# Optimization experiments

Measured on AMD Instinct MI355X. Metric: run time of the kernel, lower is better.

The kernel has to match this reference:

```python
import jax, jax.numpy as jnp
import numpy as np

FEAT_STRIDE = 16
NEG_THR, POS_THR = 0.3, 0.7        # cfg.TRAIN.RPN_NEGATIVE_OVERLAP / RPN_POSITIVE_OVERLAP
RPN_BATCHSIZE, NUM_FG = 256, 128   # RPN_BATCHSIZE, FG_FRACTION=0.5
A_PER_LOC = 9


def generate_anchors(base_size=16, ratios=(0.5, 1.0, 2.0), scales=(8, 16, 32)):
    w = h = float(base_size)
    xc = yc = 0.5 * (base_size - 1)
    size = w * h
    ws = np.round(np.sqrt(size / np.array(ratios)))
    hs = np.round(ws * np.array(ratios))
    out = []
    for wi, hi in zip(ws, hs):
        for s in scales:
            W, H = wi * s, hi * s
            out.append([xc - 0.5 * (W - 1), yc - 0.5 * (H - 1),
                        xc + 0.5 * (W - 1), yc + 0.5 * (H - 1)])
    return np.array(out, dtype=np.float32)  # [9, 4]


def _forward(rpn_cls_score, gt_boxes, im_info):
    B, _, H, W = rpn_cls_score.shape
    A = A_PER_LOC
    base = jnp.asarray(generate_anchors())
    sx, sy = jnp.meshgrid(jnp.arange(W) * FEAT_STRIDE, jnp.arange(H) * FEAT_STRIDE)  # 'xy', [H,W]
    shifts = jnp.stack([sx.ravel(), sy.ravel(), sx.ravel(), sy.ravel()], 1).astype(jnp.float32)  # [K,4]
    anchors = (base[None, :, :] + shifts[:, None, :]).reshape(-1, 4)  # [N=K*A, 4], (h,w,a)-major
    N = anchors.shape[0]

    img_h, img_w = im_info[0, 0], im_info[0, 1]
    inside = ((anchors[:, 0] >= 0) & (anchors[:, 1] >= 0) &
              (anchors[:, 2] < img_w) & (anchors[:, 3] < img_h))  # [N]

    # ---- IoU overlaps (torch +1 pixel convention) ----
    gt = gt_boxes[..., :4]  # [B,Kg,4]
    aw = anchors[:, 2] - anchors[:, 0] + 1.0
    ah = anchors[:, 3] - anchors[:, 1] + 1.0
    a_area = aw * ah                                   # [N]
    g_area = (gt[..., 2] - gt[..., 0] + 1.0) * (gt[..., 3] - gt[..., 1] + 1.0)  # [B,Kg]
    ix = jnp.maximum(0.0, jnp.minimum(anchors[None, :, None, 2], gt[:, None, :, 2])
                     - jnp.maximum(anchors[None, :, None, 0], gt[:, None, :, 0]) + 1.0)
    iy = jnp.maximum(0.0, jnp.minimum(anchors[None, :, None, 3], gt[:, None, :, 3])
                     - jnp.maximum(anchors[None, :, None, 1], gt[:, None, :, 1]) + 1.0)
    inter = ix * iy
    ovr = inter / (a_area[None, :, None] + g_area[:, None, :] - inter)  # [B,N,Kg]

    max_ovr = ovr.max(2)
    arg = ovr.argmax(2)                                 # [B,N]
    ovr_in = jnp.where(inside[None, :, None], ovr, 0.0)  # only in-image anchors compete for gt-max
    gt_max = ovr_in.max(1)                              # [B,Kg]
    gt_max = jnp.where(gt_max == 0.0, 1e-5, gt_max)
    is_best = (ovr_in == gt_max[:, None, :]).any(2)     # [B,N]

    # ---- label assignment (RPN_CLOBBER_POSITIVES = False) ----
    lbl = jnp.full((B, N), -1.0, jnp.float32)
    lbl = jnp.where(inside[None] & (max_ovr < NEG_THR), 0.0, lbl)
    lbl = jnp.where(inside[None] & is_best, 1.0, lbl)
    lbl = jnp.where(inside[None] & (max_ovr >= POS_THR), 1.0, lbl)

    # ---- random fg/bg subsampling (deterministic jax PRNG replaces np.random.permutation) ----
    def _subsample(lbl_b, key):
        kf, kb = jax.random.split(key)
        def disable(l, mask, limit, k):
            prio = jnp.where(mask, jax.random.uniform(k, l.shape), -1.0)
            order = jnp.argsort(-prio)
            rank = jnp.zeros(l.shape[0], jnp.int32).at[order].set(jnp.arange(l.shape[0], dtype=jnp.int32))
            return jnp.where(mask & (rank >= limit), -1.0, l)
        lbl_b = disable(lbl_b, lbl_b == 1.0, NUM_FG, kf)
        num_bg = RPN_BATCHSIZE - jnp.sum(lbl_b == 1.0)
        return disable(lbl_b, lbl_b == 0.0, num_bg, kb)

    lbl = jax.vmap(_subsample)(lbl, jax.random.split(jax.random.key(42), B))

    assigned = jnp.take_along_axis(gt, arg[..., None], axis=1)  # [B,N,4]
    acx = anchors[:, 0] + 0.5 * (aw - 1.0)
    acy = anchors[:, 1] + 0.5 * (ah - 1.0)
    g_w = assigned[..., 2] - assigned[..., 0] + 1.0
    g_h = assigned[..., 3] - assigned[..., 1] + 1.0
    gcx = assigned[..., 0] + 0.5 * (g_w - 1.0)
    gcy = assigned[..., 1] + 0.5 * (g_h - 1.0)
    targets = jnp.stack([(gcx - acx[None]) / aw[None], (gcy - acy[None]) / ah[None],
                         jnp.log(g_w / aw[None]), jnp.log(g_h / ah[None])], -1)  # [B,N,4]

    in_w = jnp.where(lbl == 1.0, 1.0, 0.0)             # RPN_BBOX_INSIDE_WEIGHTS = 1
    num_examples = jnp.sum(lbl >= 0.0, axis=1).astype(jnp.float32)  # RPN_POSITIVE_WEIGHT = -1
    uw = 1.0 / num_examples                             # uniform pos/neg weight, per batch
    out_w = jnp.where((lbl == 1.0) | (lbl == 0.0), uw[:, None], 0.0)

    # ---- _unmap with fill=0 for out-of-image anchors ----
    lbl = jnp.where(inside[None], lbl, 0.0)
    targets = jnp.where(inside[None, :, None], targets, 0.0)
    in_w = jnp.where(inside[None], in_w, 0.0)
    out_w = jnp.where(inside[None], out_w, 0.0)

    labels_out = lbl.reshape(B, H, W, A).transpose(0, 3, 1, 2).reshape(B, 1, A * H, W)
    targets_out = targets.reshape(B, H, W, 4 * A).transpose(0, 3, 1, 2)
    in_w_out = jnp.broadcast_to(in_w[..., None], (B, N, 4)).reshape(B, H, W, 4 * A).transpose(0, 3, 1, 2)
    out_w_out = jnp.broadcast_to(out_w[..., None], (B, N, 4)).reshape(B, H, W, 4 * A).transpose(0, 3, 1, 2)
    return labels_out, targets_out, in_w_out, out_w_out


def setup_inputs() -> dict:
    key = jax.random.key(0)
    B, A, H, W, Kg = 16, 9, 64, 64, 50
    k1, k2, k3, k4, k5 = jax.random.split(key, 5)
    rpn_cls_score = jax.random.normal(k1, (B, 2 * A, H, W), jnp.float32)
    # valid GT boxes inside a 1024x1024 image, class label in column 4
    x1 = jax.random.uniform(k2, (B, Kg)) * 800.0
    y1 = jax.random.uniform(k3, (B, Kg)) * 800.0
    w = 20.0 + jax.random.uniform(k4, (B, Kg)) * 200.0
    h = 20.0 + jax.random.uniform(k5, (B, Kg)) * 200.0
    cls = jnp.ones((B, Kg), jnp.float32)
    gt_boxes = jnp.stack([x1, y1, x1 + w, y1 + h, cls], -1)
    im_info = jnp.full((B, 2), 1024.0, jnp.float32)
    return {"rpn_cls_score": rpn_cls_score, "gt_boxes": gt_boxes, "im_info": im_info, "num_boxes": Kg}


def reference(rpn_cls_score, gt_boxes, im_info, num_boxes):
    return _forward(rpn_cls_score, gt_boxes, im_info)
```

## Files before the change

kernel.cpp:

```cpp
#include <hip/hip_runtime.h>
#include <stdint.h>


#define B_   16
#define A_   9
#define H_   64
#define W_   64
#define HW_  (H_*W_)
#define N_   (HW_*A_)
#define KG_  50
#define S0_  (B_*A_*HW_)
#define S1_  (B_*4*A_*HW_)
#define NGTB_ (B_*KG_)
#define CAP_  20480
#define NHIST_ (B_*2*256 + B_*2)

typedef unsigned long long ull;

__constant__ float c_base[A_][4] = {
  { -84.f,  -40.f,  99.f,  55.f},
  {-176.f,  -88.f, 191.f, 103.f},
  {-360.f, -184.f, 375.f, 199.f},
  { -56.f,  -56.f,  71.f,  71.f},
  {-120.f, -120.f, 135.f, 135.f},
  {-248.f, -248.f, 263.f, 263.f},
  { -36.f,  -80.f,  51.f,  95.f},
  { -80.f, -168.f,  95.f, 183.f},
  {-168.f, -344.f, 183.f, 359.f},
};

__device__ __forceinline__ void tf2x32(uint32_t k0, uint32_t k1,
                                       uint32_t x0, uint32_t x1,
                                       uint32_t& o0, uint32_t& o1) {
  const uint32_t ks2 = k0 ^ k1 ^ 0x1BD11BDAu;
  uint32_t ks[3] = {k0, k1, ks2};
  x0 += ks[0]; x1 += ks[1];
  const int R[2][4] = {{13,15,26,6},{17,29,16,24}};
  #pragma unroll
  for (int i = 0; i < 5; i++) {
    #pragma unroll
    for (int j = 0; j < 4; j++) {
      x0 += x1;
      int r = R[i & 1][j];
      x1 = (x1 << r) | (x1 >> (32 - r));
      x1 ^= x0;
    }
    x0 += ks[(i + 1) % 3];
    x1 += ks[(i + 2) % 3] + (uint32_t)(i + 1);
  }
  o0 = x0; o1 = x1;
}

__device__ __attribute__((noinline))
float box_area_f(float x1, float y1, float x2, float y2) {
#pragma clang fp contract(off)
  return (x2 - x1 + 1.f) * (y2 - y1 + 1.f);
}

__device__ __attribute__((noinline))
float iou_core(float ax1, float ay1, float ax2, float ay2, float aarea,
               float gx1, float gy1, float gx2, float gy2, float garea) {
#pragma clang fp contract(off)
  float ix = fmaxf(fminf(ax2, gx2) - fmaxf(ax1, gx1) + 1.f, 0.f);
  float iy = fmaxf(fminf(ay2, gy2) - fmaxf(ay1, gy1) + 1.f, 0.f);
  float inter = ix * iy;
  return inter / (aarea + garea - inter);
}

__global__ __launch_bounds__(256) void k_gtmax(const float* __restrict__ gtb,
                                               const float* __restrict__ iminfo,
                                               float* __restrict__ gt_max,
                                               uint32_t* __restrict__ keys,
                                               int* __restrict__ cnt_hist) {
  const int b = blockIdx.x / KG_;
  const int g = blockIdx.x % KG_;
  const int tid = threadIdx.x;
  if (blockIdx.x == 0 && tid < B_) {
    uint32_t k0, k1, kf0, kf1, kb0, kb1;
    tf2x32(0u, 42u, 0u, (uint32_t)tid, k0, k1);
    tf2x32(k0, k1, 0u, 0u, kf0, kf1);
    tf2x32(k0, k1, 0u, 1u, kb0, kb1);
    keys[tid * 4 + 0] = kf0;
    keys[tid * 4 + 1] = kf1;
    keys[tid * 4 + 2] = kb0;
    keys[tid * 4 + 3] = kb1;
  }
  if (blockIdx.x < 32) {
    const int per = (NHIST_ + 31) / 32;
    const int base = blockIdx.x * per;
    const int lim = min(base + per, NHIST_);
    for (int i = base + tid; i < lim; i += 256) cnt_hist[i] = 0;
  }
  const float* gp = gtb + (b * KG_ + g) * 5;
  const float gx1 = gp[0], gy1 = gp[1], gx2 = gp[2], gy2 = gp[3];
  const float garea = box_area_f(gx1, gy1, gx2, gy2);
  const float imh = iminfo[0], imw = iminfo[1];
  float best = 0.f;
  for (int a = 0; a < A_; a++) {
    const float bx1 = c_base[a][0], by1 = c_base[a][1];
    const float bx2 = c_base[a][2], by2 = c_base[a][3];
    const float aarea = box_area_f(bx1, by1, bx2, by2);
    int xlo = max(0, (int)ceilf(-bx1 / 16.f));
    int xhi = min(W_ - 1, (int)ceilf((imw - bx2) / 16.f) - 1);
    int ylo = max(0, (int)ceilf(-by1 / 16.f));
    int yhi = min(H_ - 1, (int)ceilf((imh - by2) / 16.f) - 1);
    xlo = max(xlo, (int)floorf((gx1 - 1.f - bx2) / 16.f));
    xhi = min(xhi, (int)ceilf((gx2 + 1.f - bx1) / 16.f));
    ylo = max(ylo, (int)floorf((gy1 - 1.f - by2) / 16.f));
    yhi = min(yhi, (int)ceilf((gy2 + 1.f - by1) / 16.f));
    const int nx = xhi - xlo + 1, ny = yhi - ylo + 1;
    if (nx <= 0 || ny <= 0) continue;
    const int lw = (nx <= 1) ? 0 : (32 - __clz(nx - 1));
    const int tot = ny << lw;
    const int mask = (1 << lw) - 1;
    for (int t = tid; t < tot; t += 256) {
      const int xi = t & mask;
      if (xi >= nx) continue;
      const int x = xlo + xi;
      const int y = ylo + (t >> lw);
      const float sx = 16.f * (float)x, sy = 16.f * (float)y;
      best = fmaxf(best, iou_core(bx1 + sx, by1 + sy, bx2 + sx, by2 + sy,
                                  aarea, gx1, gy1, gx2, gy2, garea));
    }
  }
  best = fmaxf(best, __shfl_xor(best, 32));
  best = fmaxf(best, __shfl_xor(best, 16));
  best = fmaxf(best, __shfl_xor(best, 8));
  best = fmaxf(best, __shfl_xor(best, 4));
  best = fmaxf(best, __shfl_xor(best, 2));
  best = fmaxf(best, __shfl_xor(best, 1));
  __shared__ float sw[4];
  if ((tid & 63) == 0) sw[tid >> 6] = best;
  __syncthreads();
  if (tid == 0)
    gt_max[b * KG_ + g] = fmaxf(fmaxf(sw[0], sw[1]), fmaxf(sw[2], sw[3]));
}

__global__ __launch_bounds__(256) void k_fuse(const float* __restrict__ gtb,
                                              const float* __restrict__ iminfo,
                                              const float* __restrict__ gt_max,
                                              const uint32_t* __restrict__ keys,
                                              float* __restrict__ lbl,
                                              int* __restrict__ amax,
                                              ull* __restrict__ cand,
                                              int* __restrict__ cnt,
                                              int* __restrict__ hist) {
  __shared__ float sgx1[KG_], sgy1[KG_], sgx2[KG_], sgy2[KG_], sga[KG_], sgm[KG_];
  __shared__ int s_xlo[A_], s_ylo[A_], s_nx[A_], s_pre[A_ + 1];
  __shared__ uint32_t s_k[4];
  __shared__ int s_num[2], s_base[2];
  const int b = blockIdx.y;
  const int tid = threadIdx.x;
  if (tid < KG_) {
    const float* g = gtb + (b * KG_ + tid) * 5;
    float x1 = g[0], y1 = g[1], x2 = g[2], y2 = g[3];
    sgx1[tid] = x1; sgy1[tid] = y1; sgx2[tid] = x2; sgy2[tid] = y2;
    sga[tid] = box_area_f(x1, y1, x2, y2);
    float gm = gt_max[b * KG_ + tid];
    sgm[tid] = (gm == 0.f) ? 1e-5f : gm;
  }
  if (tid < 4) s_k[tid] = keys[b * 4 + tid];
  if (tid < 2) s_num[tid] = 0;
  if (tid < A_) {
    const float imh = iminfo[0], imw = iminfo[1];
    const float bx1 = c_base[tid][0], by1 = c_base[tid][1];
    const float bx2 = c_base[tid][2], by2 = c_base[tid][3];
    int xlo = max(0, (int)ceilf(-bx1 / 16.f));
    int xhi = min(W_ - 1, (int)ceilf((imw - bx2) / 16.f) - 1);
    int ylo = max(0, (int)ceilf(-by1 / 16.f));
    int yhi = min(H_ - 1, (int)ceilf((imh - by2) / 16.f) - 1);
    int nx = max(0, xhi - xlo + 1), ny = max(0, yhi - ylo + 1);
    s_xlo[tid] = xlo; s_ylo[tid] = ylo; s_nx[tid] = nx;
    s_pre[tid + 1] = nx * ny;
  }
  __syncthreads();
  if (tid == 0) {
    s_pre[0] = 0;
    for (int a = 0; a < A_; a++) s_pre[a + 1] += s_pre[a];
  }
  __syncthreads();
  const int C = s_pre[A_];
  const int t = blockIdx.x * 256 + tid;

  bool act = false;
  int p = 0, lpos = 0, n = 0;
  uint32_t m = 0;
  if (t < C) {
    int a = 0;
    while (t >= s_pre[a + 1]) a++;
    const int idx = t - s_pre[a];
    const int nx = s_nx[a];
    const int y = s_ylo[a] + idx / nx;
    const int x = s_xlo[a] + (idx - (idx / nx) * nx);
    n = (y * W_ + x) * A_ + a;
    const float sx = 16.f * (float)x, sy = 16.f * (float)y;
    const float ax1 = c_base[a][0] + sx, ay1 = c_base[a][1] + sy;
    const float ax2 = c_base[a][2] + sx, ay2 = c_base[a][3] + sy;
    const float aarea = box_area_f(c_base[a][0], c_base[a][1],
                                   c_base[a][2], c_base[a][3]);
    float mo = -1.f;
    int bidx = 0;
    bool best = false;
    for (int k = 0; k < KG_; k++) {
      float ovr = iou_core(ax1, ay1, ax2, ay2, aarea,
                           sgx1[k], sgy1[k], sgx2[k], sgy2[k], sga[k]);
      if (ovr > mo) { mo = ovr; bidx = k; }
      best = best || (ovr == sgm[k]);
    }
    float l = -1.f;
    if (mo < 0.3f) l = 0.f;
    if (best || mo >= 0.7f) l = 1.f;
    lbl[(size_t)b * N_ + n] = l;
    amax[(size_t)b * N_ + n] = bidx;
    if (l >= 0.f) {
      act = true;
      p = (l == 1.f) ? 0 : 1;
      uint32_t y0, y1;
      tf2x32(s_k[2 * p], s_k[2 * p + 1], 0u, (uint32_t)n, y0, y1);
      m = (y0 ^ y1) >> 9;
      lpos = atomicAdd(&s_num[p], 1);
    }
  }
  __syncthreads();
  if (tid < 2 && s_num[tid] > 0)
    s_base[tid] = atomicAdd(&cnt[b * 2 + tid], s_num[tid]);
  __syncthreads();
  if (act) {
    cand[(size_t)(b * 2 + p) * CAP_ + s_base[p] + lpos] =
        ((ull)m << 16) | (ull)(65535 - n);
    atomicAdd(&hist[(b * 2 + p) * 256 + (int)(m >> 15)], 1);
  }
}

__global__ __launch_bounds__(256) void k_select(const ull* __restrict__ cand,
                                                const int* __restrict__ cnt,
                                                const int* __restrict__ hist,
                                                ull* __restrict__ Kstar,
                                                float* __restrict__ uw) {
  const int b = blockIdx.x >> 1, p = blockIdx.x & 1;
  const int tid = threadIdx.x;
  __shared__ ull s_keys[2048];
  __shared__ int s_bin, s_r, s_n;
  const int cf = cnt[b * 2 + 0], cb = cnt[b * 2 + 1];
  const int limit = (p == 0) ? 128 : 256 - min(cf, 128);
  const int c = (p == 0) ? cf : cb;
  if (p == 1 && tid == 0) {
    int kf = min(cf, 128);
    int kb = min(cb, 256 - kf);
    uw[b] = 1.f / (float)(kf + kb);
  }
  if (c <= limit) {
    if (tid == 0) Kstar[b * 2 + p] = 0ull;
    return;
  }
  if (tid == 0) {
    const int* Hh = hist + (b * 2 + p) * 256;
    int acc = 0, bin = 255, r = 0;
    for (; bin >= 0; bin--) {
      int hv = Hh[bin];
      if (acc + hv >= limit) { r = limit - acc; break; }
      acc += hv;
    }
    s_bin = bin; s_r = r; s_n = 0;
  }
  __syncthreads();
  const uint32_t bin0 = (uint32_t)s_bin;
  const int r0 = s_r;
  const ull* C = cand + (size_t)(b * 2 + p) * CAP_;
  for (int i = tid; i < c; i += 256) {
    ull k = C[i];
    if ((uint32_t)(k >> 31) == bin0) {
      int pos = atomicAdd(&s_n, 1);
      if (pos < 2048) s_keys[pos] = k;
    }
  }
  __syncthreads();
  const int s = min(s_n, 2048);
  for (int j = tid; j < s; j += 256) {
    ull kj = s_keys[j];
    int rank = 0;
    for (int q = 0; q < s; q++) rank += (s_keys[q] > kj) ? 1 : 0;
    if (rank == r0 - 1) Kstar[b * 2 + p] = kj;
  }
}

__global__ __launch_bounds__(256) void k_out(const float* __restrict__ gtb,
                                             const float* __restrict__ iminfo,
                                             const float* __restrict__ lbl,
                                             const int* __restrict__ amax,
                                             const ull* __restrict__ Kstar,
                                             const float* __restrict__ uw,
                                             const uint32_t* __restrict__ keys,
                                             float* __restrict__ out) {
  const int t = blockIdx.x * 256 + threadIdx.x;
  const int w = t & 63;
  const int h = (t >> 6) & 63;
  const int a = (t >> 12) % A_;
  const int b = t / (A_ * HW_);
  const int n = (h * W_ + w) * A_ + a;

  const float ax1 = c_base[a][0] + 16.f * (float)w;
  const float ay1 = c_base[a][1] + 16.f * (float)h;
  const float ax2 = c_base[a][2] + 16.f * (float)w;
  const float ay2 = c_base[a][3] + 16.f * (float)h;
  const float imh = iminfo[0], imw = iminfo[1];
  const bool ins = (ax1 >= 0.f) && (ay1 >= 0.f) && (ax2 < imw) && (ay2 < imh);

  float l = ins ? lbl[(size_t)b * N_ + n] : -1.f;
  if (ins && l >= 0.f) {
    const int p = (l == 1.f) ? 0 : 1;
    uint32_t y0, y1;
    tf2x32(keys[b * 4 + 2 * p], keys[b * 4 + 2 * p + 1], 0u, (uint32_t)n, y0, y1);
    ull key = ((ull)((y0 ^ y1) >> 9) << 16) | (ull)(65535 - n);
    if (key < Kstar[b * 2 + p]) l = -1.f;
  }

  out[(size_t)b * (A_ * HW_) + a * HW_ + h * W_ + w] = ins ? l : 0.f;

  float tx = 0.f, ty = 0.f, tw = 0.f, th = 0.f;
  if (ins) {
    const int g = amax[(size_t)b * N_ + n];
    const float* gp = gtb + ((size_t)b * KG_ + g) * 5;
    float aw = ax2 - ax1 + 1.f, ah = ay2 - ay1 + 1.f;
    float acx = ax1 + 0.5f * (aw - 1.f), acy = ay1 + 0.5f * (ah - 1.f);
    float gw = gp[2] - gp[0] + 1.f, gh = gp[3] - gp[1] + 1.f;
    float gcx = gp[0] + 0.5f * (gw - 1.f), gcy = gp[1] + 0.5f * (gh - 1.f);
    tx = (gcx - acx) / aw;
    ty = (gcy - acy) / ah;
    tw = logf(gw / aw);
    th = logf(gh / ah);
  }
  float* o1 = out + S0_;
  const size_t toff = (size_t)b * (4 * A_ * HW_) + (4 * a) * HW_ + h * W_ + w;
  o1[toff]           = tx;
  o1[toff + HW_]     = ty;
  o1[toff + 2 * HW_] = tw;
  o1[toff + 3 * HW_] = th;

  const float inw = (ins && l == 1.f) ? 1.f : 0.f;
  const float oww = (ins && l >= 0.f) ? uw[b] : 0.f;
  float* o2 = out + S0_ + S1_;
  o2[toff] = inw; o2[toff + HW_] = inw; o2[toff + 2 * HW_] = inw; o2[toff + 3 * HW_] = inw;
  float* o3 = out + S0_ + 2 * (size_t)S1_;
  o3[toff] = oww; o3[toff + HW_] = oww; o3[toff + 2 * HW_] = oww; o3[toff + 3 * HW_] = oww;
}

extern "C" void kernel_launch(void* const* d_in, const int* in_sizes, int n_in,
                              void* d_out, int out_size, void* d_ws, size_t ws_size,
                              hipStream_t stream) {
  const float* gtb = (const float*)d_in[1];
  const float* iminfo = (const float*)d_in[2];
  float* out = (float*)d_out;

  float* lbl = (float*)d_ws;
  int* amax = (int*)(lbl + (size_t)B_ * N_);
  float* gt_max = (float*)(amax + (size_t)B_ * N_);
  float* uw = gt_max + B_ * KG_;
  uint32_t* keys = (uint32_t*)(uw + B_);
  int* cnt = (int*)(keys + B_ * 4);
  int* hist = cnt + B_ * 2;
  ull* Kstar = (ull*)(hist + B_ * 2 * 256);
  ull* cand = Kstar + B_ * 2;

  k_gtmax<<<NGTB_, 256, 0, stream>>>(gtb, iminfo, gt_max, keys, cnt);
  k_fuse<<<dim3(144, B_), 256, 0, stream>>>(gtb, iminfo, gt_max, keys,
                                            lbl, amax, cand, cnt, hist);
  k_select<<<B_ * 2, 256, 0, stream>>>(cand, cnt, hist, Kstar, uw);
  k_out<<<S0_ / 256, 256, 0, stream>>>(gtb, iminfo, lbl, amax, Kstar, uw,
                                       keys, out);
}
```

Baseline: 137.1 us.

## Pack label and argmax into one int and vectorize output kernel with float4

Label and argmax index are packed into a single int array stored in (a,h,w) order, so the intermediate workspace is half as large and the output kernel reads it contiguously. The output kernel now handles four consecutive w positions per thread, loading an int4 and writing float4 stores to all output planes. The fuse kernel becomes a grid-stride loop with fewer blocks (73 per batch instead of 144), which adds a few extra barriers per iteration. Cost: more registers per thread in the output kernel and fewer threads in flight for the IoU stage.

```diff
diff --git a/kernel.cpp b/kernel.cpp
--- a/kernel.cpp
+++ b/kernel.cpp
@@ -140,8 +140,7 @@
                                               const float* __restrict__ iminfo,
                                               const float* __restrict__ gt_max,
                                               const uint32_t* __restrict__ keys,
-                                              float* __restrict__ lbl,
-                                              int* __restrict__ amax,
+                                              int* __restrict__ packed,
                                               ull* __restrict__ cand,
                                               int* __restrict__ cnt,
                                               int* __restrict__ hist) {
@@ -160,7 +159,6 @@
     sgm[tid] = (gm == 0.f) ? 1e-5f : gm;
   }
   if (tid < 4) s_k[tid] = keys[b * 4 + tid];
-  if (tid < 2) s_num[tid] = 0;
   if (tid < A_) {
     const float imh = iminfo[0], imw = iminfo[1];
     const float bx1 = c_base[tid][0], by1 = c_base[tid][1];
@@ -180,55 +178,61 @@
   }
   __syncthreads();
   const int C = s_pre[A_];
-  const int t = blockIdx.x * 256 + tid;
-
-  bool act = false;
-  int p = 0, lpos = 0, n = 0;
-  uint32_t m = 0;
-  if (t < C) {
-    int a = 0;
-    while (t >= s_pre[a + 1]) a++;
-    const int idx = t - s_pre[a];
-    const int nx = s_nx[a];
-    const int y = s_ylo[a] + idx / nx;
-    const int x = s_xlo[a] + (idx - (idx / nx) * nx);
-    n = (y * W_ + x) * A_ + a;
-    const float sx = 16.f * (float)x, sy = 16.f * (float)y;
-    const float ax1 = c_base[a][0] + sx, ay1 = c_base[a][1] + sy;
-    const float ax2 = c_base[a][2] + sx, ay2 = c_base[a][3] + sy;
-    const float aarea = box_area_f(c_base[a][0], c_base[a][1],
-                                   c_base[a][2], c_base[a][3]);
-    float mo = -1.f;
-    int bidx = 0;
-    bool best = false;
-    for (int k = 0; k < KG_; k++) {
-      float ovr = iou_core(ax1, ay1, ax2, ay2, aarea,
-                           sgx1[k], sgy1[k], sgx2[k], sgy2[k], sga[k]);
-      if (ovr > mo) { mo = ovr; bidx = k; }
-      best = best || (ovr == sgm[k]);
-    }
-    float l = -1.f;
-    if (mo < 0.3f) l = 0.f;
-    if (best || mo >= 0.7f) l = 1.f;
-    lbl[(size_t)b * N_ + n] = l;
-    amax[(size_t)b * N_ + n] = bidx;
-    if (l >= 0.f) {
-      act = true;
-      p = (l == 1.f) ? 0 : 1;
-      uint32_t y0, y1;
-      tf2x32(s_k[2 * p], s_k[2 * p + 1], 0u, (uint32_t)n, y0, y1);
-      m = (y0 ^ y1) >> 9;
-      lpos = atomicAdd(&s_num[p], 1);
-    }
-  }
-  __syncthreads();
-  if (tid < 2 && s_num[tid] > 0)
-    s_base[tid] = atomicAdd(&cnt[b * 2 + tid], s_num[tid]);
-  __syncthreads();
-  if (act) {
-    cand[(size_t)(b * 2 + p) * CAP_ + s_base[p] + lpos] =
-        ((ull)m << 16) | (ull)(65535 - n);
-    atomicAdd(&hist[(b * 2 + p) * 256 + (int)(m >> 15)], 1);
+  const int stride = gridDim.x * 256;
+
+  for (int t0 = blockIdx.x * 256; t0 < C; t0 += stride) {
+    if (tid < 2) s_num[tid] = 0;
+    __syncthreads();
+    const int t = t0 + tid;
+    bool act = false;
+    int p = 0, lpos = 0, n = 0;
+    uint32_t m = 0;
+    if (t < C) {
+      int a = 0;
+      while (t >= s_pre[a + 1]) a++;
+      const int idx = t - s_pre[a];
+      const int nx = s_nx[a];
+      const int y = s_ylo[a] + idx / nx;
+      const int x = s_xlo[a] + (idx - (idx / nx) * nx);
+      n = (y * W_ + x) * A_ + a;
+      const int n2 = a * HW_ + y * W_ + x;
+      const float sx = 16.f * (float)x, sy = 16.f * (float)y;
+      const float ax1 = c_base[a][0] + sx, ay1 = c_base[a][1] + sy;
+      const float ax2 = c_base[a][2] + sx, ay2 = c_base[a][3] + sy;
+      const float aarea = box_area_f(c_base[a][0], c_base[a][1],
+                                     c_base[a][2], c_base[a][3]);
+      float mo = -1.f;
+      int bidx = 0;
+      bool best = false;
+      for (int k = 0; k < KG_; k++) {
+        float ovr = iou_core(ax1, ay1, ax2, ay2, aarea,
+                             sgx1[k], sgy1[k], sgx2[k], sgy2[k], sga[k]);
+        if (ovr > mo) { mo = ovr; bidx = k; }
+        best = best || (ovr == sgm[k]);
+      }
+      int lab = -1;
+      if (mo < 0.3f) lab = 0;
+      if (best || mo >= 0.7f) lab = 1;
+      packed[(size_t)b * N_ + n2] = (bidx << 2) | (lab + 1);
+      if (lab >= 0) {
+        act = true;
+        p = (lab == 1) ? 0 : 1;
+        uint32_t y0, y1;
+        tf2x32(s_k[2 * p], s_k[2 * p + 1], 0u, (uint32_t)n, y0, y1);
+        m = (y0 ^ y1) >> 9;
+        lpos = atomicAdd(&s_num[p], 1);
+      }
+    }
+    __syncthreads();
+    if (tid < 2 && s_num[tid] > 0)
+      s_base[tid] = atomicAdd(&cnt[b * 2 + tid], s_num[tid]);
+    __syncthreads();
+    if (act) {
+      cand[(size_t)(b * 2 + p) * CAP_ + s_base[p] + lpos] =
+          ((ull)m << 16) | (ull)(65535 - n);
+      atomicAdd(&hist[(b * 2 + p) * 256 + (int)(m >> 15)], 1);
+    }
+    __syncthreads();
   }
 }
 
@@ -286,63 +290,88 @@
 
 __global__ __launch_bounds__(256) void k_out(const float* __restrict__ gtb,
                                              const float* __restrict__ iminfo,
-                                             const float* __restrict__ lbl,
-                                             const int* __restrict__ amax,
+                                             const int* __restrict__ packed,
                                              const ull* __restrict__ Kstar,
                                              const float* __restrict__ uw,
                                              const uint32_t* __restrict__ keys,
                                              float* __restrict__ out) {
-  const int t = blockIdx.x * 256 + threadIdx.x;
-  const int w = t & 63;
-  const int h = (t >> 6) & 63;
-  const int a = (t >> 12) % A_;
-  const int b = t / (A_ * HW_);
-  const int n = (h * W_ + w) * A_ + a;
-
-  const float ax1 = c_base[a][0] + 16.f * (float)w;
+  const int gid = blockIdx.x * 256 + threadIdx.x;
+  const int e = gid * 4;
+  const int w0 = e & 63;
+  const int h = (e >> 6) & 63;
+  const int a = (e >> 12) % A_;
+  const int b = e / (A_ * HW_);
+
+  const float imh = iminfo[0], imw = iminfo[1];
   const float ay1 = c_base[a][1] + 16.f * (float)h;
-  const float ax2 = c_base[a][2] + 16.f * (float)w;
   const float ay2 = c_base[a][3] + 16.f * (float)h;
-  const float imh = iminfo[0], imw = iminfo[1];
-  const bool ins = (ax1 >= 0.f) && (ay1 >= 0.f) && (ax2 < imw) && (ay2 < imh);
-
-  float l = ins ? lbl[(size_t)b * N_ + n] : -1.f;
-  if (ins && l >= 0.f) {
-    const int p = (l == 1.f) ? 0 : 1;
-    uint32_t y0, y1;
-    tf2x32(keys[b * 4 + 2 * p], keys[b * 4 + 2 * p + 1], 0u, (uint32_t)n, y0, y1);
-    ull key = ((ull)((y0 ^ y1) >> 9) << 16) | (ull)(65535 - n);
-    if (key < Kstar[b * 2 + p]) l = -1.f;
-  }
-
-  out[(size_t)b * (A_ * HW_) + a * HW_ + h * W_ + w] = ins ? l : 0.f;
-
-  float tx = 0.f, ty = 0.f, tw = 0.f, th = 0.f;
-  if (ins) {
-    const int g = amax[(size_t)b * N_ + n];
-    const float* gp = gtb + ((size_t)b * KG_ + g) * 5;
-    float aw = ax2 - ax1 + 1.f, ah = ay2 - ay1 + 1.f;
-    float acx = ax1 + 0.5f * (aw - 1.f), acy = ay1 + 0.5f * (ah - 1.f);
-    float gw = gp[2] - gp[0] + 1.f, gh = gp[3] - gp[1] + 1.f;
-    float gcx = gp[0] + 0.5f * (gw - 1.f), gcy = gp[1] + 0.5f * (gh - 1.f);
-    tx = (gcx - acx) / aw;
-    ty = (gcy - acy) / ah;
-    tw = logf(gw / aw);
-    th = logf(gh / ah);
-  }
+  const bool insY = (ay1 >= 0.f) && (ay2 < imh);
+
+  const int4 pk4 = *(const int4*)(packed + e);
+  const int pk[4] = {pk4.x, pk4.y, pk4.z, pk4.w};
+  const float uwb = uw[b];
+  const ull KF_ = Kstar[b * 2 + 0];
+  const ull KB_ = Kstar[b * 2 + 1];
+  const uint32_t kf0 = keys[b * 4 + 0], kf1 = keys[b * 4 + 1];
+  const uint32_t kb0 = keys[b * 4 + 2], kb1 = keys[b * 4 + 3];
+
+  float4 lab4, tx4, ty4, tw4, th4, inw4, oww4;
+  float* labp = (float*)&lab4;
+  float* txp = (float*)&tx4; float* typ = (float*)&ty4;
+  float* twp = (float*)&tw4; float* thp = (float*)&th4;
+  float* inwp = (float*)&inw4; float* owwp = (float*)&oww4;
+
+  #pragma unroll
+  for (int j = 0; j < 4; j++) {
+    const int w = w0 + j;
+    const float ax1 = c_base[a][0] + 16.f * (float)w;
+    const float ax2 = c_base[a][2] + 16.f * (float)w;
+    const bool ins = insY && (ax1 >= 0.f) && (ax2 < imw);
+    int lab = (pk[j] & 3) - 1;
+    const int g = pk[j] >> 2;
+    float tx = 0.f, ty = 0.f, tw = 0.f, th = 0.f;
+    if (ins) {
+      if (lab >= 0) {
+        const int n = (h * W_ + w) * A_ + a;
+        const int p = (lab == 1) ? 0 : 1;
+        uint32_t y0, y1;
+        tf2x32(p ? kb0 : kf0, p ? kb1 : kf1, 0u, (uint32_t)n, y0, y1);
+        ull key = ((ull)((y0 ^ y1) >> 9) << 16) | (ull)(65535 - n);
+        if (key < (p ? KB_ : KF_)) lab = -1;
+      }
+      const float* gp = gtb + ((size_t)b * KG_ + g) * 5;
+      float aw = ax2 - ax1 + 1.f, ah = ay2 - ay1 + 1.f;
+      float acx = ax1 + 0.5f * (aw - 1.f), acy = ay1 + 0.5f * (ah - 1.f);
+      float gw = gp[2] - gp[0] + 1.f, gh = gp[3] - gp[1] + 1.f;
+      float gcx = gp[0] + 0.5f * (gw - 1.f), gcy = gp[1] + 0.5f * (gh - 1.f);
+      tx = (gcx - acx) / aw;
+      ty = (gcy - acy) / ah;
+      tw = logf(gw / aw);
+      th = logf(gh / ah);
+    }
+    labp[j] = ins ? (float)lab : 0.f;
+    txp[j] = tx; typ[j] = ty; twp[j] = tw; thp[j] = th;
+    inwp[j] = (ins && lab == 1) ? 1.f : 0.f;
+    owwp[j] = (ins && lab >= 0) ? uwb : 0.f;
+  }
+
+  *(float4*)(out + e) = lab4;
   float* o1 = out + S0_;
-  const size_t toff = (size_t)b * (4 * A_ * HW_) + (4 * a) * HW_ + h * W_ + w;
-  o1[toff]           = tx;
-  o1[toff + HW_]     = ty;
-  o1[toff + 2 * HW_] = tw;
-  o1[toff + 3 * HW_] = th;
-
-  const float inw = (ins && l == 1.f) ? 1.f : 0.f;
-  const float oww = (ins && l >= 0.f) ? uw[b] : 0.f;
+  const size_t toff = (size_t)b * (4 * A_ * HW_) + (4 * a) * HW_ + h * W_ + w0;
+  *(float4*)(o1 + toff)           = tx4;
+  *(float4*)(o1 + toff + HW_)     = ty4;
+  *(float4*)(o1 + toff + 2 * HW_) = tw4;
+  *(float4*)(o1 + toff + 3 * HW_) = th4;
   float* o2 = out + S0_ + S1_;
-  o2[toff] = inw; o2[toff + HW_] = inw; o2[toff + 2 * HW_] = inw; o2[toff + 3 * HW_] = inw;
+  *(float4*)(o2 + toff)           = inw4;
+  *(float4*)(o2 + toff + HW_)     = inw4;
+  *(float4*)(o2 + toff + 2 * HW_) = inw4;
+  *(float4*)(o2 + toff + 3 * HW_) = inw4;
   float* o3 = out + S0_ + 2 * (size_t)S1_;
-  o3[toff] = oww; o3[toff + HW_] = oww; o3[toff + 2 * HW_] = oww; o3[toff + 3 * HW_] = oww;
+  *(float4*)(o3 + toff)           = oww4;
+  *(float4*)(o3 + toff + HW_)     = oww4;
+  *(float4*)(o3 + toff + 2 * HW_) = oww4;
+  *(float4*)(o3 + toff + 3 * HW_) = oww4;
 }
 
 extern "C" void kernel_launch(void* const* d_in, const int* in_sizes, int n_in,
@@ -352,9 +381,8 @@
   const float* iminfo = (const float*)d_in[2];
   float* out = (float*)d_out;
 
-  float* lbl = (float*)d_ws;
-  int* amax = (int*)(lbl + (size_t)B_ * N_);
-  float* gt_max = (float*)(amax + (size_t)B_ * N_);
+  int* packed = (int*)d_ws;
+  float* gt_max = (float*)(packed + (size_t)B_ * N_);
   float* uw = gt_max + B_ * KG_;
   uint32_t* keys = (uint32_t*)(uw + B_);
   int* cnt = (int*)(keys + B_ * 4);
@@ -363,9 +391,9 @@
   ull* cand = Kstar + B_ * 2;
 
   k_gtmax<<<NGTB_, 256, 0, stream>>>(gtb, iminfo, gt_max, keys, cnt);
-  k_fuse<<<dim3(144, B_), 256, 0, stream>>>(gtb, iminfo, gt_max, keys,
-                                            lbl, amax, cand, cnt, hist);
+  k_fuse<<<dim3(73, B_), 256, 0, stream>>>(gtb, iminfo, gt_max, keys,
+                                           packed, cand, cnt, hist);
   k_select<<<B_ * 2, 256, 0, stream>>>(cand, cnt, hist, Kstar, uw);
-  k_out<<<S0_ / 256, 256, 0, stream>>>(gtb, iminfo, lbl, amax, Kstar, uw,
-                                       keys, out);
-}
+  k_out<<<S0_ / 4 / 256, 256, 0, stream>>>(gtb, iminfo, packed, Kstar, uw,
+                                           keys, out);
+}
```

Result: no change. 137.1 us (median of 2 runs) (-0.1%).
